# Kernel optimization log

Measured on AMD Instinct MI355X. Metric: run time of the kernel, lower is better.

The kernel has to match this reference:

```python
import jax, jax.numpy as jnp
import numpy as np

HIDDEN = 256
HEAD_DIM = 256
SCALE_BASE = 512
SEQ_LEN = 243
CHUNK = 81
NUM_JOINTS = 17
BATCH = 64
GAMMA = [0.9, 0.91, 0.92, 0.93, 0.94, 0.95, 0.955, 0.96, 0.965, 0.97,
         0.975, 0.98, 0.985, 0.99, 0.992, 0.994, 0.996]


def duplicate_interleave(m):
    # (L, d/2) -> (L, d), each element repeated twice along last dim
    return jnp.repeat(m, 2, axis=-1)


def rotate_every_two(x):
    x1 = x[..., ::2]
    x2 = x[..., 1::2]
    return jnp.stack((-x2, x1), axis=-1).reshape(x.shape)


def xpos(x, downscale=False):
    # x: (B, L, head_dim); offset = 0
    L = x.shape[1]
    half = HEAD_DIM // 2
    base_scale = (jnp.arange(0, HEAD_DIM, 2, dtype=jnp.float32) + 0.4 * HEAD_DIM) / (1.4 * HEAD_DIM)  # (half,)
    pos = jnp.arange(L, dtype=jnp.float32)
    scale = base_scale[None, :] ** (pos / SCALE_BASE)[:, None]  # (L, half)
    # fixed_pos_embedding on `scale` (seq_len=L, dim=half)
    inv_freq = 1.0 / 10000.0 ** (jnp.arange(half, dtype=jnp.float32) / half)
    sinusoid = pos[:, None] * inv_freq[None, :]  # (L, half)
    sin, cos = jnp.sin(sinusoid), jnp.cos(sinusoid)
    if downscale:
        scale = 1.0 / scale
    sin_s = duplicate_interleave(sin * scale)  # (L, head_dim)
    cos_s = duplicate_interleave(cos * scale)
    return x * cos_s[None] + rotate_every_two(x) * sin_s[None]


def decay_mask(gamma):
    # (J, L, L): D[k, i, j] = gamma_k ** |i - j| for j < end-of-chunk(i), else 0
    i = jnp.arange(SEQ_LEN)[:, None]
    j = jnp.arange(SEQ_LEN)[None, :]
    allowed = j < (i // CHUNK + 1) * CHUNK  # (L, L)
    absdiff = jnp.abs(i - j).astype(jnp.float32)
    D = gamma[:, None, None] ** absdiff[None]  # (J, L, L)
    D = jnp.where(allowed[None], D, 0.0)
    return jnp.where(jnp.isnan(D), 0.0, D)


def setup_inputs() -> dict:
    key = jax.random.key(0)
    k0, k1, k2, k3 = jax.random.split(key, 4)
    X = jax.random.normal(k0, (BATCH * NUM_JOINTS, SEQ_LEN, HIDDEN), jnp.float32)
    W_Q = jax.random.normal(k1, (HIDDEN, HEAD_DIM), jnp.float32) / HIDDEN
    W_K = jax.random.normal(k2, (HIDDEN, HEAD_DIM), jnp.float32) / HIDDEN
    W_V = jax.random.normal(k3, (HIDDEN, HEAD_DIM), jnp.float32) / HIDDEN
    gamma = jnp.asarray(GAMMA, jnp.float32)
    return {"X": X, "W_Q": W_Q, "W_K": W_K, "W_V": W_V, "gamma": gamma}


def reference(X, W_Q, W_K, W_V, gamma):
    L = X.shape[1]
    Q = xpos(X @ W_Q)                      # (B*J, L, d)
    K = xpos(X @ W_K, downscale=True)      # (B*J, L, d)
    V = X @ W_V                            # (B*J, L, v)
    D = decay_mask(gamma)                  # (J, L, L)
    ret = jnp.einsum('bld,bmd->blm', Q, K)              # (B*J, L, L)
    ret = ret.reshape(-1, NUM_JOINTS, L, L) * D[None]   # apply per-joint decay mask
    ret = ret.reshape(-1, L, L)
    return ret @ V                          # (B*J, L, v)
```

## Files before the change

### kernel.cpp

```cpp
#include <hip/hip_runtime.h>
#include <stdint.h>

#define L_SEQ 243
#define HID   256
#define CHK   81
#define NJ    17
#define NB    1088

typedef short bf16x8 __attribute__((ext_vector_type(8)));
typedef float f32x4  __attribute__((ext_vector_type(4)));

__device__ __forceinline__ unsigned short f2bf(float f) {
  unsigned int u = __float_as_uint(f);
  u = (u + 0x7fffu + ((u >> 16) & 1u)) >> 16;
  return (unsigned short)u;
}

#define OFF_Q   0ull
#define OFF_K   135364608ull
#define OFF_V   270729216ull
#define OFF_WT  408879104ull
#define OFF_TAB 409272320ull
#define OFF_GP  409769984ull
#define WS_NEED 409787392ull

__global__ void prep_kernel(const float* __restrict__ Wq, const float* __restrict__ Wk,
                            const float* __restrict__ Wv, const float* __restrict__ gamma,
                            unsigned short* __restrict__ Wt,
                            float* __restrict__ cu, float* __restrict__ su,
                            float* __restrict__ cd, float* __restrict__ sd,
                            float* __restrict__ gp) {
  int id = blockIdx.x * 256 + threadIdx.x;
  if (id < 768 * 256) {
    int n = id >> 8, k = id & 255;
    const float* W = (n < 256) ? Wq : (n < 512 ? Wk : Wv);
    Wt[n * 256 + k] = f2bf(W[k * 256 + (n & 255)]);
  } else if (id < 768 * 256 + L_SEQ * 128) {
    int r = id - 768 * 256;
    int p = r >> 7, h = r & 127;
    float base  = (2.0f * h + 102.4f) / 358.4f;
    float scale = powf(base, (float)p * (1.0f / 512.0f));
    float invf  = powf(10000.0f, -(float)h * (1.0f / 128.0f));
    float ang   = (float)p * invf;
    float s, c; sincosf(ang, &s, &c);
    cu[p * 128 + h] = c * scale;  su[p * 128 + h] = s * scale;
    cd[p * 128 + h] = c / scale;  sd[p * 128 + h] = s / scale;
  } else if (id < 768 * 256 + L_SEQ * 128 + NJ * 256) {
    int r = id - (768 * 256 + L_SEQ * 128);
    int j = r >> 8, d = r & 255;
    gp[r] = (d < L_SEQ) ? powf(gamma[j], (float)d) : 0.0f;
  }
}

__global__ __launch_bounds__(256, 2)
void proj_kernel(const float* __restrict__ X, const unsigned short* __restrict__ Wt,
                 const float* __restrict__ cu, const float* __restrict__ su,
                 const float* __restrict__ cd, const float* __restrict__ sd,
                 unsigned short* __restrict__ Qw, unsigned short* __restrict__ Kw,
                 unsigned short* __restrict__ Vt) {
  __shared__ __align__(16) unsigned short Xs[128 * 264];
  __shared__ __align__(16) unsigned short Ws[128 * 40];
  int tid = threadIdx.x;
  int gid = blockIdx.x;
  int b = gid % NB, mt = gid / NB;
  int m0 = mt * 128;
  int wid = tid >> 6, lane = tid & 63, ln = lane & 15, quad = lane >> 4;
  int mw = (wid >> 1) * 64, nw = (wid & 1) * 64;
  const float* Xb = X + (size_t)b * (L_SEQ * HID);

  for (int it = 0; it < 32; ++it) {
    int idx = it * 256 + tid;
    int r = idx >> 6, c4 = (idx & 63) << 2;
    int p = m0 + r;
    float4 v = make_float4(0.f, 0.f, 0.f, 0.f);
    if (p < L_SEQ) v = *(const float4*)(Xb + p * HID + c4);
    ushort4 h;
    h.x = f2bf(v.x); h.y = f2bf(v.y); h.z = f2bf(v.z); h.w = f2bf(v.w);
    *(ushort4*)&Xs[r * 264 + c4] = h;
  }

  for (int nt = 0; nt < 6; ++nt) {
    int n0 = nt * 128;
    f32x4 acc[4][4] = {};
    for (int ks = 0; ks < 8; ++ks) {
      __syncthreads();
      for (int it = 0; it < 2; ++it) {
        int idx = it * 256 + tid;
        int r = idx >> 2, seg = idx & 3;
        uint4 w = *(const uint4*)(Wt + (n0 + r) * 256 + ks * 32 + seg * 8);
        *(uint4*)&Ws[r * 40 + seg * 8] = w;
      }
      __syncthreads();
      bf16x8 a[4], bb[4];
      for (int t = 0; t < 4; ++t)
        a[t] = *(const bf16x8*)&Xs[(mw + 16 * t + ln) * 264 + ks * 32 + quad * 8];
      for (int t = 0; t < 4; ++t)
        bb[t] = *(const bf16x8*)&Ws[(nw + 16 * t + ln) * 40 + quad * 8];
      for (int i = 0; i < 4; ++i)
        for (int j = 0; j < 4; ++j)
          acc[i][j] = __builtin_amdgcn_mfma_f32_16x16x32_bf16(a[i], bb[j], acc[i][j], 0, 0, 0);
    }
    if (nt < 4) {
      bool isQ = (nt < 2);
      const float* ct = isQ ? cu : cd;
      const float* st = isQ ? su : sd;
      unsigned short* Dst = isQ ? Qw : Kw;
      for (int i = 0; i < 4; ++i) {
        int pb = m0 + mw + 16 * i + quad * 4;
        for (int j = 0; j < 4; ++j) {
          int n = n0 + nw + 16 * j + ln;
          int d = n & 255, h = d >> 1;
          for (int r = 0; r < 4; ++r) {
            float v  = acc[i][j][r];
            float pv = __shfl_xor(v, 1, 64);
            int pp = pb + r;
            int tp = (pp < L_SEQ) ? pp : 0;
            float c = ct[tp * 128 + h], s = st[tp * 128 + h];
            float o = (d & 1) ? (v * c + pv * s) : (v * c - pv * s);
            if (pp < L_SEQ) Dst[((size_t)b * L_SEQ + pp) * 256 + d] = f2bf(o);
          }
        }
      }
    } else {
      for (int i = 0; i < 4; ++i) {
        int p0 = m0 + mw + 16 * i + quad * 4;
        for (int j = 0; j < 4; ++j) {
          int d = (n0 - 512) + nw + 16 * j + ln;
          ushort4 pk;
          pk.x = f2bf(acc[i][j][0]); pk.y = f2bf(acc[i][j][1]);
          pk.z = f2bf(acc[i][j][2]); pk.w = f2bf(acc[i][j][3]);
          size_t base = ((size_t)b * 256 + d) * 248 + p0;
          if (p0 + 3 < L_SEQ) {
            *(ushort4*)(Vt + base) = pk;
          } else {
            unsigned short tmp[4] = {pk.x, pk.y, pk.z, pk.w};
            for (int r = 0; r < 4; ++r) if (p0 + r < L_SEQ) Vt[base + r] = tmp[r];
          }
        }
      }
    }
  }
}

__global__ __launch_bounds__(256, 2)
void attn_kernel(const unsigned short* __restrict__ Qw, const unsigned short* __restrict__ Kw,
                 const unsigned short* __restrict__ Vt, const float* __restrict__ gpow,
                 float* __restrict__ Out) {
  __shared__ __align__(16) unsigned short Qs[64 * 264];
  __shared__ __align__(16) unsigned short Ks[32 * 264];
  __shared__ __align__(16) unsigned short Vts[256 * 40];
  __shared__ __align__(16) unsigned short Ps[64 * 40];
  __shared__ float gp[256];
  int tid = threadIdx.x;
  int gid = blockIdx.x;
  int b = gid % NB, qb = gid / NB;
  int wid = tid >> 6, lane = tid & 63, ln = lane & 15, quad = lane >> 4;

  gp[tid] = gpow[(b % NJ) * 256 + tid];

  for (int it = 0; it < 8; ++it) {
    int idx = it * 256 + tid;
    int r = idx >> 5, seg = idx & 31;
    int p = qb * 64 + r;
    uint4 v = make_uint4(0, 0, 0, 0);
    if (p < L_SEQ) v = *(const uint4*)(Qw + ((size_t)b * L_SEQ + p) * 256 + seg * 8);
    *(uint4*)&Qs[r * 264 + seg * 8] = v;
  }

  f32x4 o[16] = {};
  for (int kb = 0; kb < 8; ++kb) {
    int m0 = kb * 32;
    __syncthreads();
    for (int it = 0; it < 4; ++it) {
      int idx = it * 256 + tid;
      int r = idx >> 5, seg = idx & 31;
      int p = m0 + r;
      uint4 v = make_uint4(0, 0, 0, 0);
      if (p < L_SEQ) v = *(const uint4*)(Kw + ((size_t)b * L_SEQ + p) * 256 + seg * 8);
      *(uint4*)&Ks[r * 264 + seg * 8] = v;
    }
    for (int it = 0; it < 4; ++it) {
      int idx = it * 256 + tid;
      int r = idx >> 2, seg = idx & 3;
      int p0 = m0 + seg * 8;
      const unsigned short* src = Vt + ((size_t)b * 256 + r) * 248 + p0;
      uint4 v;
      if (p0 + 8 <= L_SEQ) {
        v = *(const uint4*)src;
      } else {
        union { unsigned short u[8]; uint4 v4; } tt;
        for (int e = 0; e < 8; ++e) tt.u[e] = (p0 + e < L_SEQ) ? src[e] : 0;
        v = tt.v4;
      }
      *(uint4*)&Vts[r * 40 + seg * 8] = v;
    }
    __syncthreads();
    f32x4 s[2] = {};
    for (int ks = 0; ks < 8; ++ks) {
      bf16x8 aq = *(const bf16x8*)&Qs[(wid * 16 + ln) * 264 + ks * 32 + quad * 8];
      for (int t = 0; t < 2; ++t) {
        bf16x8 bk = *(const bf16x8*)&Ks[(t * 16 + ln) * 264 + ks * 32 + quad * 8];
        s[t] = __builtin_amdgcn_mfma_f32_16x16x32_bf16(aq, bk, s[t], 0, 0, 0);
      }
    }
    for (int t = 0; t < 2; ++t) {
      int m = m0 + t * 16 + ln;
      for (int r = 0; r < 4; ++r) {
        int iloc = wid * 16 + quad * 4 + r;
        int i = qb * 64 + iloc;
        int lim = (i / CHK + 1) * CHK; if (lim > L_SEQ) lim = L_SEQ;
        int ad = (i > m) ? (i - m) : (m - i);
        float f = (m < lim) ? gp[ad] : 0.0f;
        Ps[iloc * 40 + t * 16 + ln] = f2bf(s[t][r] * f);
      }
    }
    __syncthreads();
    bf16x8 ap = *(const bf16x8*)&Ps[(wid * 16 + ln) * 40 + quad * 8];
    for (int nt = 0; nt < 16; ++nt) {
      bf16x8 bv = *(const bf16x8*)&Vts[(nt * 16 + ln) * 40 + quad * 8];
      o[nt] = __builtin_amdgcn_mfma_f32_16x16x32_bf16(ap, bv, o[nt], 0, 0, 0);
    }
  }
  for (int nt = 0; nt < 16; ++nt) {
    int d = nt * 16 + ln;
    for (int r = 0; r < 4; ++r) {
      int p = qb * 64 + wid * 16 + quad * 4 + r;
      if (p < L_SEQ) Out[((size_t)b * L_SEQ + p) * 256 + d] = o[nt][r];
    }
  }
}

extern "C" void kernel_launch(void* const* d_in, const int* in_sizes, int n_in,
                              void* d_out, int out_size, void* d_ws, size_t ws_size,
                              hipStream_t stream) {
  const float* X     = (const float*)d_in[0];
  const float* Wq    = (const float*)d_in[1];
  const float* Wk    = (const float*)d_in[2];
  const float* Wv    = (const float*)d_in[3];
  const float* gamma = (const float*)d_in[4];
  if (ws_size < WS_NEED) return;

  char* ws = (char*)d_ws;
  unsigned short* Qw  = (unsigned short*)(ws + OFF_Q);
  unsigned short* Kw  = (unsigned short*)(ws + OFF_K);
  unsigned short* Vtw = (unsigned short*)(ws + OFF_V);
  unsigned short* Wt  = (unsigned short*)(ws + OFF_WT);
  float* cu = (float*)(ws + OFF_TAB);
  float* su = cu + L_SEQ * 128;
  float* cd = su + L_SEQ * 128;
  float* sd = cd + L_SEQ * 128;
  float* gp = (float*)(ws + OFF_GP);

  hipLaunchKernelGGL(prep_kernel, dim3(907), dim3(256), 0, stream,
                     Wq, Wk, Wv, gamma, Wt, cu, su, cd, sd, gp);
  hipLaunchKernelGGL(proj_kernel, dim3(2176), dim3(256), 0, stream,
                     X, Wt, cu, su, cd, sd, Qw, Kw, Vtw);
  hipLaunchKernelGGL(attn_kernel, dim3(4352), dim3(256), 0, stream,
                     Qw, Kw, Vtw, gp, (float*)d_out);
}
```

Measured before the change: 1.366 ms.

## Drop LDS staging for weights/K/V, shrink proj tile, skip masked key blocks

The projection kernel now uses 64-row tiles with each wave owning 64 output columns, and reads weight fragments straight from global memory instead of staging them in LDS behind barriers. This doubles the grid and raises the occupancy hint. The attention kernel keeps Q fragments in registers and loads K and V^T fragments directly from global memory per wave. Each wave keeps only a private P tile in LDS, so per-block barriers go away. It also stops iterating over key blocks beyond the chunk causal limit, and the V^T padding columns are now zeroed. The cost is more global or L2 traffic with no LDS reuse of K/V across waves, plus higher register pressure.

Measured after the change: 1.795 ms. +31.4%, slower.

```diff
diff --git a/kernel.cpp b/kernel.cpp
--- a/kernel.cpp
+++ b/kernel.cpp
@@ -52,89 +52,100 @@
   }
 }
 
-__global__ __launch_bounds__(256, 2)
+__global__ __launch_bounds__(256, 4)
 void proj_kernel(const float* __restrict__ X, const unsigned short* __restrict__ Wt,
                  const float* __restrict__ cu, const float* __restrict__ su,
                  const float* __restrict__ cd, const float* __restrict__ sd,
                  unsigned short* __restrict__ Qw, unsigned short* __restrict__ Kw,
                  unsigned short* __restrict__ Vt) {
-  __shared__ __align__(16) unsigned short Xs[128 * 264];
-  __shared__ __align__(16) unsigned short Ws[128 * 40];
+  __shared__ __align__(16) unsigned short Xs[64 * 264];
   int tid = threadIdx.x;
   int gid = blockIdx.x;
   int b = gid % NB, mt = gid / NB;
-  int m0 = mt * 128;
+  int m0 = mt * 64;
   int wid = tid >> 6, lane = tid & 63, ln = lane & 15, quad = lane >> 4;
-  int mw = (wid >> 1) * 64, nw = (wid & 1) * 64;
   const float* Xb = X + (size_t)b * (L_SEQ * HID);
 
-  for (int it = 0; it < 32; ++it) {
+  #pragma unroll
+  for (int it = 0; it < 8; ++it) {
     int idx = it * 256 + tid;
-    int r = idx >> 6, c4 = (idx & 63) << 2;
+    int r = idx >> 5, seg = idx & 31;
     int p = m0 + r;
-    float4 v = make_float4(0.f, 0.f, 0.f, 0.f);
-    if (p < L_SEQ) v = *(const float4*)(Xb + p * HID + c4);
-    ushort4 h;
-    h.x = f2bf(v.x); h.y = f2bf(v.y); h.z = f2bf(v.z); h.w = f2bf(v.w);
-    *(ushort4*)&Xs[r * 264 + c4] = h;
-  }
-
-  for (int nt = 0; nt < 6; ++nt) {
-    int n0 = nt * 128;
+    float4 v0 = make_float4(0.f, 0.f, 0.f, 0.f), v1 = v0;
+    if (p < L_SEQ) {
+      v0 = *(const float4*)(Xb + p * HID + seg * 8);
+      v1 = *(const float4*)(Xb + p * HID + seg * 8 + 4);
+    }
+    union { unsigned short u[8]; uint4 v; } pk;
+    pk.u[0] = f2bf(v0.x); pk.u[1] = f2bf(v0.y); pk.u[2] = f2bf(v0.z); pk.u[3] = f2bf(v0.w);
+    pk.u[4] = f2bf(v1.x); pk.u[5] = f2bf(v1.y); pk.u[6] = f2bf(v1.z); pk.u[7] = f2bf(v1.w);
+    *(uint4*)&Xs[r * 264 + seg * 8] = pk.v;
+  }
+  __syncthreads();
+
+  for (int nt = 0; nt < 3; ++nt) {
     f32x4 acc[4][4] = {};
+    int nb0 = nt * 256 + wid * 64;
+    #pragma unroll
     for (int ks = 0; ks < 8; ++ks) {
-      __syncthreads();
-      for (int it = 0; it < 2; ++it) {
-        int idx = it * 256 + tid;
-        int r = idx >> 2, seg = idx & 3;
-        uint4 w = *(const uint4*)(Wt + (n0 + r) * 256 + ks * 32 + seg * 8);
-        *(uint4*)&Ws[r * 40 + seg * 8] = w;
-      }
-      __syncthreads();
-      bf16x8 a[4], bb[4];
-      for (int t = 0; t < 4; ++t)
-        a[t] = *(const bf16x8*)&Xs[(mw + 16 * t + ln) * 264 + ks * 32 + quad * 8];
-      for (int t = 0; t < 4; ++t)
-        bb[t] = *(const bf16x8*)&Ws[(nw + 16 * t + ln) * 40 + quad * 8];
+      bf16x8 a[4], bw[4];
+      #pragma unroll
+      for (int j = 0; j < 4; ++j)
+        bw[j] = *(const bf16x8*)(Wt + (nb0 + 16 * j + ln) * 256 + ks * 32 + quad * 8);
+      #pragma unroll
       for (int i = 0; i < 4; ++i)
+        a[i] = *(const bf16x8*)&Xs[(16 * i + ln) * 264 + ks * 32 + quad * 8];
+      #pragma unroll
+      for (int i = 0; i < 4; ++i)
+        #pragma unroll
         for (int j = 0; j < 4; ++j)
-          acc[i][j] = __builtin_amdgcn_mfma_f32_16x16x32_bf16(a[i], bb[j], acc[i][j], 0, 0, 0);
-    }
-    if (nt < 4) {
-      bool isQ = (nt < 2);
-      const float* ct = isQ ? cu : cd;
-      const float* st = isQ ? su : sd;
-      unsigned short* Dst = isQ ? Qw : Kw;
+          acc[i][j] = __builtin_amdgcn_mfma_f32_16x16x32_bf16(a[i], bw[j], acc[i][j], 0, 0, 0);
+    }
+    if (nt < 2) {
+      const float* ct = (nt == 0) ? cu : cd;
+      const float* st = (nt == 0) ? su : sd;
+      unsigned short* Dst = (nt == 0) ? Qw : Kw;
+      #pragma unroll
       for (int i = 0; i < 4; ++i) {
-        int pb = m0 + mw + 16 * i + quad * 4;
+        int pb = m0 + 16 * i + quad * 4;
+        #pragma unroll
         for (int j = 0; j < 4; ++j) {
-          int n = n0 + nw + 16 * j + ln;
-          int d = n & 255, h = d >> 1;
+          int d = wid * 64 + 16 * j + ln;
+          int h = d >> 1;
+          #pragma unroll
           for (int r = 0; r < 4; ++r) {
             float v  = acc[i][j][r];
             float pv = __shfl_xor(v, 1, 64);
-            int pp = pb + r;
-            int tp = (pp < L_SEQ) ? pp : 0;
-            float c = ct[tp * 128 + h], s = st[tp * 128 + h];
-            float o = (d & 1) ? (v * c + pv * s) : (v * c - pv * s);
-            if (pp < L_SEQ) Dst[((size_t)b * L_SEQ + pp) * 256 + d] = f2bf(o);
+            int p = pb + r;
+            if (p < L_SEQ) {
+              float c = ct[p * 128 + h], s = st[p * 128 + h];
+              float o = (d & 1) ? (v * c + pv * s) : (v * c - pv * s);
+              Dst[((size_t)b * L_SEQ + p) * 256 + d] = f2bf(o);
+            }
           }
         }
       }
     } else {
+      #pragma unroll
       for (int i = 0; i < 4; ++i) {
-        int p0 = m0 + mw + 16 * i + quad * 4;
+        int p0 = m0 + 16 * i + quad * 4;
+        #pragma unroll
         for (int j = 0; j < 4; ++j) {
-          int d = (n0 - 512) + nw + 16 * j + ln;
-          ushort4 pk;
-          pk.x = f2bf(acc[i][j][0]); pk.y = f2bf(acc[i][j][1]);
-          pk.z = f2bf(acc[i][j][2]); pk.w = f2bf(acc[i][j][3]);
+          int d = wid * 64 + 16 * j + ln;
           size_t base = ((size_t)b * 256 + d) * 248 + p0;
           if (p0 + 3 < L_SEQ) {
+            ushort4 pk;
+            pk.x = f2bf(acc[i][j][0]); pk.y = f2bf(acc[i][j][1]);
+            pk.z = f2bf(acc[i][j][2]); pk.w = f2bf(acc[i][j][3]);
             *(ushort4*)(Vt + base) = pk;
-          } else {
-            unsigned short tmp[4] = {pk.x, pk.y, pk.z, pk.w};
-            for (int r = 0; r < 4; ++r) if (p0 + r < L_SEQ) Vt[base + r] = tmp[r];
+          } else if (p0 < 248) {
+            #pragma unroll
+            for (int r = 0; r < 4; ++r) {
+              if (p0 + r < 248) {
+                unsigned short val = (p0 + r < L_SEQ) ? f2bf(acc[i][j][r]) : (unsigned short)0;
+                Vt[base + r] = val;
+              }
+            }
           }
         }
       }
@@ -142,87 +153,82 @@
   }
 }
 
-__global__ __launch_bounds__(256, 2)
+__global__ __launch_bounds__(256, 3)
 void attn_kernel(const unsigned short* __restrict__ Qw, const unsigned short* __restrict__ Kw,
                  const unsigned short* __restrict__ Vt, const float* __restrict__ gpow,
                  float* __restrict__ Out) {
-  __shared__ __align__(16) unsigned short Qs[64 * 264];
-  __shared__ __align__(16) unsigned short Ks[32 * 264];
-  __shared__ __align__(16) unsigned short Vts[256 * 40];
-  __shared__ __align__(16) unsigned short Ps[64 * 40];
-  __shared__ float gp[256];
+  __shared__ __align__(16) unsigned short Ps[4 * 16 * 40];
+  __shared__ float gps[256];
   int tid = threadIdx.x;
   int gid = blockIdx.x;
   int b = gid % NB, qb = gid / NB;
   int wid = tid >> 6, lane = tid & 63, ln = lane & 15, quad = lane >> 4;
 
-  gp[tid] = gpow[(b % NJ) * 256 + tid];
-
-  for (int it = 0; it < 8; ++it) {
-    int idx = it * 256 + tid;
-    int r = idx >> 5, seg = idx & 31;
-    int p = qb * 64 + r;
-    uint4 v = make_uint4(0, 0, 0, 0);
-    if (p < L_SEQ) v = *(const uint4*)(Qw + ((size_t)b * L_SEQ + p) * 256 + seg * 8);
-    *(uint4*)&Qs[r * 264 + seg * 8] = v;
-  }
+  gps[tid] = gpow[(b % NJ) * 256 + tid];
+
+  int qrow = qb * 64 + wid * 16 + ln;
+  int qr = (qrow < L_SEQ) ? qrow : (L_SEQ - 1);
+  const unsigned short* Qp = Qw + ((size_t)b * L_SEQ + qr) * 256 + quad * 8;
+  bf16x8 aq[8];
+  #pragma unroll
+  for (int ks = 0; ks < 8; ++ks) aq[ks] = *(const bf16x8*)(Qp + ks * 32);
+
+  int i0 = qb * 64 + wid * 16 + quad * 4;
+  int lim[4];
+  #pragma unroll
+  for (int r = 0; r < 4; ++r) {
+    int l = ((i0 + r) / CHK + 1) * CHK;
+    lim[r] = (l > L_SEQ) ? L_SEQ : l;
+  }
+  int lmax = ((qb * 64 + 63) / CHK + 1) * CHK;
+  if (lmax > L_SEQ) lmax = L_SEQ;
+  int nkb = (lmax + 31) >> 5;
+
+  const unsigned short* Kb = Kw + (size_t)b * (L_SEQ * 256);
+  const unsigned short* Vb = Vt + (size_t)b * (256 * 248);
+  unsigned short* Pw = &Ps[wid * 640];
+
+  __syncthreads();
 
   f32x4 o[16] = {};
-  for (int kb = 0; kb < 8; ++kb) {
+  for (int kb = 0; kb < nkb; ++kb) {
     int m0 = kb * 32;
-    __syncthreads();
-    for (int it = 0; it < 4; ++it) {
-      int idx = it * 256 + tid;
-      int r = idx >> 5, seg = idx & 31;
-      int p = m0 + r;
-      uint4 v = make_uint4(0, 0, 0, 0);
-      if (p < L_SEQ) v = *(const uint4*)(Kw + ((size_t)b * L_SEQ + p) * 256 + seg * 8);
-      *(uint4*)&Ks[r * 264 + seg * 8] = v;
-    }
-    for (int it = 0; it < 4; ++it) {
-      int idx = it * 256 + tid;
-      int r = idx >> 2, seg = idx & 3;
-      int p0 = m0 + seg * 8;
-      const unsigned short* src = Vt + ((size_t)b * 256 + r) * 248 + p0;
-      uint4 v;
-      if (p0 + 8 <= L_SEQ) {
-        v = *(const uint4*)src;
-      } else {
-        union { unsigned short u[8]; uint4 v4; } tt;
-        for (int e = 0; e < 8; ++e) tt.u[e] = (p0 + e < L_SEQ) ? src[e] : 0;
-        v = tt.v4;
+    int k0 = m0 + ln, k1 = m0 + 16 + ln;
+    int kr0 = (k0 < L_SEQ) ? k0 : (L_SEQ - 1);
+    int kr1 = (k1 < L_SEQ) ? k1 : (L_SEQ - 1);
+    const unsigned short* Kp0 = Kb + (size_t)kr0 * 256 + quad * 8;
+    const unsigned short* Kp1 = Kb + (size_t)kr1 * 256 + quad * 8;
+    f32x4 s0 = {}, s1 = {};
+    #pragma unroll
+    for (int ks = 0; ks < 8; ++ks) {
+      bf16x8 bk0 = *(const bf16x8*)(Kp0 + ks * 32);
+      bf16x8 bk1 = *(const bf16x8*)(Kp1 + ks * 32);
+      s0 = __builtin_amdgcn_mfma_f32_16x16x32_bf16(aq[ks], bk0, s0, 0, 0, 0);
+      s1 = __builtin_amdgcn_mfma_f32_16x16x32_bf16(aq[ks], bk1, s1, 0, 0, 0);
+    }
+    #pragma unroll
+    for (int t = 0; t < 2; ++t) {
+      f32x4 sv = t ? s1 : s0;
+      int m = m0 + t * 16 + ln;
+      #pragma unroll
+      for (int r = 0; r < 4; ++r) {
+        int ad = i0 + r - m; ad = (ad < 0) ? -ad : ad;
+        float f = (m < lim[r]) ? gps[ad] : 0.0f;
+        Pw[(quad * 4 + r) * 40 + t * 16 + ln] = f2bf(sv[r] * f);
       }
-      *(uint4*)&Vts[r * 40 + seg * 8] = v;
-    }
-    __syncthreads();
-    f32x4 s[2] = {};
-    for (int ks = 0; ks < 8; ++ks) {
-      bf16x8 aq = *(const bf16x8*)&Qs[(wid * 16 + ln) * 264 + ks * 32 + quad * 8];
-      for (int t = 0; t < 2; ++t) {
-        bf16x8 bk = *(const bf16x8*)&Ks[(t * 16 + ln) * 264 + ks * 32 + quad * 8];
-        s[t] = __builtin_amdgcn_mfma_f32_16x16x32_bf16(aq, bk, s[t], 0, 0, 0);
-      }
-    }
-    for (int t = 0; t < 2; ++t) {
-      int m = m0 + t * 16 + ln;
-      for (int r = 0; r < 4; ++r) {
-        int iloc = wid * 16 + quad * 4 + r;
-        int i = qb * 64 + iloc;
-        int lim = (i / CHK + 1) * CHK; if (lim > L_SEQ) lim = L_SEQ;
-        int ad = (i > m) ? (i - m) : (m - i);
-        float f = (m < lim) ? gp[ad] : 0.0f;
-        Ps[iloc * 40 + t * 16 + ln] = f2bf(s[t][r] * f);
-      }
-    }
-    __syncthreads();
-    bf16x8 ap = *(const bf16x8*)&Ps[(wid * 16 + ln) * 40 + quad * 8];
+    }
+    bf16x8 ap = *(const bf16x8*)&Pw[ln * 40 + quad * 8];
+    const unsigned short* Vp = Vb + m0 + quad * 8;
+    #pragma unroll
     for (int nt = 0; nt < 16; ++nt) {
-      bf16x8 bv = *(const bf16x8*)&Vts[(nt * 16 + ln) * 40 + quad * 8];
+      bf16x8 bv = *(const bf16x8*)(Vp + (nt * 16 + ln) * 248);
       o[nt] = __builtin_amdgcn_mfma_f32_16x16x32_bf16(ap, bv, o[nt], 0, 0, 0);
     }
   }
+  #pragma unroll
   for (int nt = 0; nt < 16; ++nt) {
     int d = nt * 16 + ln;
+    #pragma unroll
     for (int r = 0; r < 4; ++r) {
       int p = qb * 64 + wid * 16 + quad * 4 + r;
       if (p < L_SEQ) Out[((size_t)b * L_SEQ + p) * 256 + d] = o[nt][r];
@@ -253,7 +259,7 @@
 
   hipLaunchKernelGGL(prep_kernel, dim3(907), dim3(256), 0, stream,
                      Wq, Wk, Wv, gamma, Wt, cu, su, cd, sd, gp);
-  hipLaunchKernelGGL(proj_kernel, dim3(2176), dim3(256), 0, stream,
+  hipLaunchKernelGGL(proj_kernel, dim3(4352), dim3(256), 0, stream,
                      X, Wt, cu, su, cd, sd, Qw, Kw, Vtw);
   hipLaunchKernelGGL(attn_kernel, dim3(4352), dim3(256), 0, stream,
                      Qw, Kw, Vtw, gp, (float*)d_out);
```
